# Optimization experiments

Hardware: AMD Instinct MI355X
Metric: run time of the kernel (lower is better)

The kernel has to match this reference:

```python
import jax, jax.numpy as jnp
import numpy as np

HIDDEN = 128
N_HEADS = 8
SEQ = 4096


def setup_inputs() -> dict:
    key = jax.random.key(0)
    ks = jax.random.split(key, 7)
    H, NH = HIDDEN, N_HEADS
    s = 1.0 / np.sqrt(H)
    return {
        "x": jax.random.normal(ks[0], (SEQ, H), dtype=jnp.float32),
        "W1": jax.random.uniform(ks[1], (H, H * NH), jnp.float32, -s, s),
        "b1": jax.random.uniform(ks[2], (H * NH,), jnp.float32, -s, s),
        "W2": jax.random.uniform(ks[3], (H, H * NH), jnp.float32, -s, s),
        "b2": jax.random.uniform(ks[4], (H * NH,), jnp.float32, -s, s),
        "Wc": jax.random.uniform(ks[5], (H * NH, H), jnp.float32, -1.0 / np.sqrt(H * NH), 1.0 / np.sqrt(H * NH)),
        "bc": jax.random.uniform(ks[6], (H,), jnp.float32, -1.0 / np.sqrt(H * NH), 1.0 / np.sqrt(H * NH)),
    }


def reference(x, W1, b1, W2, b2, Wc, bc):
    S, H = x.shape
    NH = W1.shape[1] // H
    # project then split into heads: [S, NH*H] -> [NH, S, H]
    q1 = (x @ W1 + b1).reshape(S, NH, H).transpose(1, 0, 2)
    q2 = (x @ W2 + b2).reshape(S, NH, H).transpose(1, 0, 2)
    # unscaled attention scores per head: [NH, S, S]
    att = jax.nn.softmax(jnp.einsum('hse,hte->hst', q1, q2), axis=-1)
    # weighted sum of q2 (values == q2 in this module): [NH, S, H]
    ctx = jnp.einsum('hst,hte->hse', att, q2)
    # concat heads back along feature dim: [S, NH*H]
    ctx = ctx.transpose(1, 0, 2).reshape(S, NH * H)
    return ctx @ Wc + bc + x
```

## Files before the change

### kernel.cpp

```cpp
#include <hip/hip_runtime.h>

#define H 128
#define NHEADS 8
#define SQ 4096
#define HD 1024

typedef float f32x4 __attribute__((ext_vector_type(4)));
typedef __bf16 bf16x8 __attribute__((ext_vector_type(8)));
typedef unsigned short u16x4 __attribute__((ext_vector_type(4)));
typedef unsigned short u16x8 __attribute__((ext_vector_type(8)));

static __device__ __forceinline__ unsigned short f2bf(float f) {
  unsigned int u = __builtin_bit_cast(unsigned int, f);
  u += 0x7fffu + ((u >> 16) & 1u);
  return (unsigned short)(u >> 16);
}
static __device__ __forceinline__ float b2f(unsigned short s) {
  unsigned int u = (unsigned int)s << 16;
  return __builtin_bit_cast(float, u);
}
static __device__ __forceinline__ bf16x8 ld_bf8(const unsigned short* p) {
  return __builtin_bit_cast(bf16x8, *(const u16x8*)p);
}

__global__ __launch_bounds__(256) void prep_kernel(
    const float* __restrict__ W1, const float* __restrict__ W2,
    const float* __restrict__ Wc,
    unsigned short* __restrict__ W1T, unsigned short* __restrict__ W2T,
    unsigned short* __restrict__ WcT)
{
  __shared__ unsigned short tile[64 * 66];
  const int b = blockIdx.x, tid = threadIdx.x;
  if (b < 32) {
    const int k0 = (b & 1) * 64, n0 = (b >> 1) * 64;
    for (int i = 0; i < 16; ++i) {
      int idx = tid + i * 256;
      int r = idx >> 6, cc = idx & 63;
      tile[cc * 66 + r] = f2bf(W1[(size_t)(k0 + r) * HD + n0 + cc]);
    }
    __syncthreads();
    for (int i = 0; i < 16; ++i) {
      int idx = tid + i * 256;
      int r = idx >> 6, cc = idx & 63;
      W1T[(size_t)(n0 + r) * H + k0 + cc] = tile[r * 66 + cc];
    }
    __syncthreads();
    for (int i = 0; i < 16; ++i) {
      int idx = tid + i * 256;
      int r = idx >> 6, cc = idx & 63;
      tile[cc * 66 + r] = f2bf(W2[(size_t)(k0 + r) * HD + n0 + cc]);
    }
    __syncthreads();
    for (int i = 0; i < 16; ++i) {
      int idx = tid + i * 256;
      int r = idx >> 6, cc = idx & 63;
      W2T[(size_t)(n0 + r) * H + k0 + cc] = tile[r * 66 + cc];
    }
  } else {
    const int bb = b - 32;
    const int n0 = (bb & 1) * 64, k0 = (bb >> 1) * 64;
    for (int i = 0; i < 16; ++i) {
      int idx = tid + i * 256;
      int r = idx >> 6, cc = idx & 63;
      tile[cc * 66 + r] = f2bf(Wc[(size_t)(k0 + r) * H + n0 + cc]);
    }
    __syncthreads();
    for (int i = 0; i < 16; ++i) {
      int idx = tid + i * 256;
      int r = idx >> 6, cc = idx & 63;
      WcT[(size_t)(n0 + r) * HD + k0 + cc] = tile[r * 66 + cc];
    }
  }
}

__global__ __launch_bounds__(256) void proj_kernel(
    const float* __restrict__ x,
    const float* __restrict__ b1, const float* __restrict__ b2,
    const unsigned short* __restrict__ W1T, const unsigned short* __restrict__ W2T,
    unsigned short* __restrict__ q1bf, unsigned short* __restrict__ q2K,
    unsigned short* __restrict__ q2VT)
{
  __shared__ unsigned short At[64 * 136];
  __shared__ unsigned short Bt[128 * 136];
  const int tid = threadIdx.x;
  const int st = blockIdx.x & 63, h = blockIdx.x >> 6;
  const int s0 = st * 64;
  const int lane = tid & 63, w = tid >> 6;
  const int c = lane & 15, q4 = lane >> 4;

  for (int i = 0; i < 4; ++i) {
    int ch = tid + i * 256;
    int row = ch >> 4, col8 = (ch & 15) * 8;
    const float* gp = x + (s0 + row) * H + col8;
    f32x4 a = *(const f32x4*)gp;
    f32x4 b = *(const f32x4*)(gp + 4);
    u16x8 v;
    v[0]=f2bf(a[0]); v[1]=f2bf(a[1]); v[2]=f2bf(a[2]); v[3]=f2bf(a[3]);
    v[4]=f2bf(b[0]); v[5]=f2bf(b[1]); v[6]=f2bf(b[2]); v[7]=f2bf(b[3]);
    *(u16x8*)&At[row * 136 + col8] = v;
  }
  for (int i = 0; i < 8; ++i) {
    int ch = tid + i * 256;
    int row = ch >> 4, col8 = (ch & 15) * 8;
    *(u16x8*)&Bt[row * 136 + col8] = *(const u16x8*)&W1T[(h * H + row) * H + col8];
  }
  __syncthreads();

  bf16x8 af[4];
  for (int kc = 0; kc < 4; ++kc)
    af[kc] = ld_bf8(&At[(w * 16 + c) * 136 + kc * 32 + q4 * 8]);
  __syncthreads();

  for (int nt = 0; nt < 8; ++nt) {
    f32x4 acc = {0.f, 0.f, 0.f, 0.f};
    for (int kc = 0; kc < 4; ++kc) {
      bf16x8 bf = ld_bf8(&Bt[(nt * 16 + c) * 136 + kc * 32 + q4 * 8]);
      acc = __builtin_amdgcn_mfma_f32_16x16x32_bf16(af[kc], bf, acc, 0, 0, 0);
    }
    float bb = b1[h * H + nt * 16 + c];
    for (int r = 0; r < 4; ++r)
      At[(w * 16 + q4 * 4 + r) * 136 + nt * 16 + c] = f2bf(acc[r] + bb);
  }
  __syncthreads();

  for (int i = 0; i < 4; ++i) {
    int ch = tid + i * 256;
    int row = ch >> 4, col8 = (ch & 15) * 8;
    *(u16x8*)&q1bf[(size_t)(h * SQ + s0 + row) * H + col8] =
        *(const u16x8*)&At[row * 136 + col8];
  }
  for (int i = 0; i < 8; ++i) {
    int ch = tid + i * 256;
    int row = ch >> 4, col8 = (ch & 15) * 8;
    *(u16x8*)&Bt[row * 136 + col8] = *(const u16x8*)&W2T[(h * H + row) * H + col8];
  }
  __syncthreads();

  f32x4 q2a[8];
  for (int nt = 0; nt < 8; ++nt) {
    f32x4 acc = {0.f, 0.f, 0.f, 0.f};
    for (int kc = 0; kc < 4; ++kc) {
      bf16x8 bf = ld_bf8(&Bt[(nt * 16 + c) * 136 + kc * 32 + q4 * 8]);
      acc = __builtin_amdgcn_mfma_f32_16x16x32_bf16(af[kc], bf, acc, 0, 0, 0);
    }
    q2a[nt] = acc;
  }
  __syncthreads();

  for (int nt = 0; nt < 8; ++nt) {
    float bb = b2[h * H + nt * 16 + c];
    unsigned short vs[4];
    for (int r = 0; r < 4; ++r) {
      unsigned short u = f2bf(q2a[nt][r] + bb);
      At[(w * 16 + q4 * 4 + r) * 136 + nt * 16 + c] = u;
      vs[r] = u;
    }
    u16x4 v4 = {vs[0], vs[1], vs[2], vs[3]};
    *(u16x4*)&Bt[(nt * 16 + c) * 72 + w * 16 + q4 * 4] = v4;
  }
  __syncthreads();

  for (int i = 0; i < 4; ++i) {
    int ch = tid + i * 256;
    int row = ch >> 4, col8 = (ch & 15) * 8;
    *(u16x8*)&q2K[(size_t)(h * SQ + s0 + row) * H + col8] =
        *(const u16x8*)&At[row * 136 + col8];
  }
  for (int i = 0; i < 4; ++i) {
    int ch = tid + i * 256;
    int row = ch >> 3, col8 = (ch & 7) * 8;
    *(u16x8*)&q2VT[(size_t)(h * H + row) * SQ + s0 + col8] =
        *(const u16x8*)&Bt[row * 72 + col8];
  }
}

__global__ __launch_bounds__(256, 2) void flash_kernel(
    const unsigned short* __restrict__ q1bf,
    const unsigned short* __restrict__ q2K,
    const unsigned short* __restrict__ q2VT,
    unsigned short* __restrict__ ctxp,
    float* __restrict__ lbuf)
{
  __shared__ unsigned short Kt[64 * 152];
  __shared__ unsigned short VT[128 * 88];
  __shared__ unsigned short Pb[4][2][16 * 72];
  const int tid = threadIdx.x;
  const int bid = blockIdx.x;
  const int kb = bid >> 8;
  const int h = (bid >> 5) & 7, qb = bid & 31;
  const int s0 = qb * 128;
  const int kbase = kb * 2048;
  const int lane = tid & 63, w = tid >> 6;
  const int c = lane & 15, q4 = lane >> 4;

  bf16x8 qf[2][4];
  for (int blk = 0; blk < 2; ++blk)
    for (int kc = 0; kc < 4; ++kc)
      qf[blk][kc] = ld_bf8(
          &q1bf[(h * SQ + s0 + w * 32 + blk * 16 + c) * H + kc * 32 + q4 * 8]);

  f32x4 acc[2][8];
  for (int blk = 0; blk < 2; ++blk)
    for (int nt = 0; nt < 8; ++nt) acc[blk][nt] = (f32x4){0.f, 0.f, 0.f, 0.f};
  float lsum[2] = {0.f, 0.f};

  u16x8 kreg[4], vreg[4];
  for (int i = 0; i < 4; ++i) {
    int ch = tid + i * 256;
    kreg[i] = *(const u16x8*)&q2K[(h * SQ + kbase + (ch >> 4)) * H + (ch & 15) * 8];
    vreg[i] = *(const u16x8*)&q2VT[(h * H + (ch >> 3)) * SQ + kbase + (ch & 7) * 8];
  }

  for (int kt = 0; kt < 32; ++kt) {
    if (kt) __syncthreads();
    for (int i = 0; i < 4; ++i) {
      int ch = tid + i * 256;
      *(u16x8*)&Kt[(ch >> 4) * 152 + (ch & 15) * 8] = kreg[i];
      *(u16x8*)&VT[(ch >> 3) * 88 + (ch & 7) * 8] = vreg[i];
    }
    __syncthreads();

    if (kt < 31) {
      const int k0 = kbase + (kt + 1) * 64;
      for (int i = 0; i < 4; ++i) {
        int ch = tid + i * 256;
        kreg[i] = *(const u16x8*)&q2K[(h * SQ + k0 + (ch >> 4)) * H + (ch & 15) * 8];
        vreg[i] = *(const u16x8*)&q2VT[(h * H + (ch >> 3)) * SQ + k0 + (ch & 7) * 8];
      }
    }

    f32x4 sc[2][4];
    for (int mt = 0; mt < 4; ++mt) {
      bf16x8 kf[4];
      for (int kc = 0; kc < 4; ++kc)
        kf[kc] = ld_bf8(&Kt[(mt * 16 + c) * 152 + kc * 32 + q4 * 8]);
      for (int blk = 0; blk < 2; ++blk) {
        f32x4 s = {0.f, 0.f, 0.f, 0.f};
        for (int kc = 0; kc < 4; ++kc)
          s = __builtin_amdgcn_mfma_f32_16x16x32_bf16(kf[kc], qf[blk][kc], s, 0, 0, 0);
        sc[blk][mt] = s;
      }
    }

    for (int blk = 0; blk < 2; ++blk) {
      float ts = 0.f;
      for (int mt = 0; mt < 4; ++mt) {
        f32x4 p;
        for (int r = 0; r < 4; ++r) { p[r] = __expf(sc[blk][mt][r]); ts += p[r]; }
        sc[blk][mt] = p;
      }
      lsum[blk] += ts;
      for (int mt = 0; mt < 4; ++mt) {
        u16x4 pv = {f2bf(sc[blk][mt][0]), f2bf(sc[blk][mt][1]),
                    f2bf(sc[blk][mt][2]), f2bf(sc[blk][mt][3])};
        *(u16x4*)&Pb[w][blk][c * 72 + mt * 16 + q4 * 4] = pv;
      }
    }

    for (int kc2 = 0; kc2 < 2; ++kc2) {
      bf16x8 pf0 = ld_bf8(&Pb[w][0][c * 72 + kc2 * 32 + q4 * 8]);
      bf16x8 pf1 = ld_bf8(&Pb[w][1][c * 72 + kc2 * 32 + q4 * 8]);
      for (int nt = 0; nt < 8; ++nt) {
        bf16x8 vf = ld_bf8(&VT[(nt * 16 + c) * 88 + kc2 * 32 + q4 * 8]);
        acc[0][nt] = __builtin_amdgcn_mfma_f32_16x16x32_bf16(pf0, vf, acc[0][nt], 0, 0, 0);
        acc[1][nt] = __builtin_amdgcn_mfma_f32_16x16x32_bf16(pf1, vf, acc[1][nt], 0, 0, 0);
      }
    }
  }

  unsigned short* ctxk = ctxp + (size_t)kb * SQ * HD;
  for (int blk = 0; blk < 2; ++blk) {
    float l = lsum[blk];
    l += __shfl_xor(l, 16);
    l += __shfl_xor(l, 32);
    float rl = 1.f / l;
    if (q4 == 0)
      lbuf[(size_t)kb * NHEADS * SQ + h * SQ + s0 + w * 32 + blk * 16 + c] = l;
    float r0 = __shfl(rl, q4 * 4 + 0);
    float r1 = __shfl(rl, q4 * 4 + 1);
    float r2 = __shfl(rl, q4 * 4 + 2);
    float r3 = __shfl(rl, q4 * 4 + 3);
    for (int nt = 0; nt < 8; ++nt) {
      int col = h * H + nt * 16 + c;
      int srow = s0 + w * 32 + blk * 16 + q4 * 4;
      ctxk[(size_t)(srow + 0) * HD + col] = f2bf(acc[blk][nt][0] * r0);
      ctxk[(size_t)(srow + 1) * HD + col] = f2bf(acc[blk][nt][1] * r1);
      ctxk[(size_t)(srow + 2) * HD + col] = f2bf(acc[blk][nt][2] * r2);
      ctxk[(size_t)(srow + 3) * HD + col] = f2bf(acc[blk][nt][3] * r3);
    }
  }
}

__global__ __launch_bounds__(256) void out_kernel(
    const unsigned short* __restrict__ ctxp,
    const float* __restrict__ lbuf,
    const unsigned short* __restrict__ WcT,
    const float* __restrict__ bc,
    const float* __restrict__ x,
    float* __restrict__ out)
{
  __shared__ unsigned short At[64 * 136];
  __shared__ unsigned short Bt[128 * 136];
  const int tid = threadIdx.x;
  const int s0 = blockIdx.x * 64;
  const int lane = tid & 63, w = tid >> 6;
  const int c = lane & 15, q4 = lane >> 4;

  f32x4 acc[8];
  for (int nt = 0; nt < 8; ++nt) acc[nt] = (f32x4){0.f, 0.f, 0.f, 0.f};

  for (int kt = 0; kt < 8; ++kt) {
    __syncthreads();
    for (int i = 0; i < 4; ++i) {
      int ch = tid + i * 256;
      int row = ch >> 4, col8 = (ch & 15) * 8;
      const unsigned short* p0 = &ctxp[(size_t)(s0 + row) * HD + kt * 128 + col8];
      u16x8 a0 = *(const u16x8*)p0;
      u16x8 a1 = *(const u16x8*)(p0 + (size_t)SQ * HD);
      float la = lbuf[(size_t)kt * SQ + s0 + row];
      float lb = lbuf[(size_t)NHEADS * SQ + (size_t)kt * SQ + s0 + row];
      float ri = 1.f / (la + lb);
      float wa = la * ri, wb = lb * ri;
      u16x8 av;
      for (int e = 0; e < 8; ++e)
        av[e] = f2bf(wa * b2f(a0[e]) + wb * b2f(a1[e]));
      *(u16x8*)&At[row * 136 + col8] = av;
    }
    for (int i = 0; i < 8; ++i) {
      int ch = tid + i * 256;
      int row = ch >> 4, col8 = (ch & 15) * 8;
      *(u16x8*)&Bt[row * 136 + col8] =
          *(const u16x8*)&WcT[row * HD + kt * 128 + col8];
    }
    __syncthreads();
    bf16x8 af[4];
    for (int kc = 0; kc < 4; ++kc)
      af[kc] = ld_bf8(&At[(w * 16 + c) * 136 + kc * 32 + q4 * 8]);
    for (int nt = 0; nt < 8; ++nt) {
      f32x4 a = acc[nt];
      for (int kc = 0; kc < 4; ++kc) {
        bf16x8 bf = ld_bf8(&Bt[(nt * 16 + c) * 136 + kc * 32 + q4 * 8]);
        a = __builtin_amdgcn_mfma_f32_16x16x32_bf16(af[kc], bf, a, 0, 0, 0);
      }
      acc[nt] = a;
    }
  }
  for (int nt = 0; nt < 8; ++nt) {
    float bb = bc[nt * 16 + c];
    for (int r = 0; r < 4; ++r) {
      int srow = s0 + w * 16 + q4 * 4 + r;
      int col = nt * 16 + c;
      out[srow * H + col] = acc[nt][r] + bb + x[srow * H + col];
    }
  }
}

extern "C" void kernel_launch(void* const* d_in, const int* in_sizes, int n_in,
                              void* d_out, int out_size, void* d_ws, size_t ws_size,
                              hipStream_t stream) {
  const float* x  = (const float*)d_in[0];
  const float* W1 = (const float*)d_in[1];
  const float* b1 = (const float*)d_in[2];
  const float* W2 = (const float*)d_in[3];
  const float* b2 = (const float*)d_in[4];
  const float* Wc = (const float*)d_in[5];
  const float* bc = (const float*)d_in[6];
  float* out = (float*)d_out;

  char* ws = (char*)d_ws;
  unsigned short* q1bf = (unsigned short*)ws; ws += (size_t)NHEADS * SQ * H * 2;
  unsigned short* q2K  = (unsigned short*)ws; ws += (size_t)NHEADS * SQ * H * 2;
  unsigned short* q2VT = (unsigned short*)ws; ws += (size_t)NHEADS * SQ * H * 2;
  unsigned short* ctxp = (unsigned short*)ws; ws += (size_t)2 * SQ * HD * 2;
  float*          lbuf = (float*)ws;          ws += (size_t)2 * NHEADS * SQ * 4;
  unsigned short* W1T  = (unsigned short*)ws; ws += (size_t)HD * H * 2;
  unsigned short* W2T  = (unsigned short*)ws; ws += (size_t)HD * H * 2;
  unsigned short* WcT  = (unsigned short*)ws; ws += (size_t)HD * H * 2;

  prep_kernel<<<64, 256, 0, stream>>>(W1, W2, Wc, W1T, W2T, WcT);
  proj_kernel<<<512, 256, 0, stream>>>(x, b1, b2, W1T, W2T, q1bf, q2K, q2VT);
  flash_kernel<<<512, 256, 0, stream>>>(q1bf, q2K, q2VT, ctxp, lbuf);
  out_kernel<<<64, 256, 0, stream>>>(ctxp, lbuf, WcT, bc, x, out);
}
```

Baseline: 207.1 us.

## Split flash attention keys into three chunks when workspace allows

The flash kernel is templated on the number of key splits. When the workspace is large enough it launches 768 blocks, with each block covering 21 or 22 key tiles, instead of 512 blocks covering 32 tiles each. The output kernel combines the NKB partial results using weights taken from the per-split row sums. LDS row padding is also reduced (152 to 136 for K, 88 to 72 for V), which can change bank conflicts. The extra split adds more partial-context traffic to global memory and more combine work in the output stage.

```diff
diff --git a/kernel.cpp b/kernel.cpp
--- a/kernel.cpp
+++ b/kernel.cpp
@@ -174,22 +174,25 @@
   }
 }
 
-__global__ __launch_bounds__(256, 2) void flash_kernel(
+template<int NKB>
+__global__ __launch_bounds__(256, NKB) void flash_kernel(
     const unsigned short* __restrict__ q1bf,
     const unsigned short* __restrict__ q2K,
     const unsigned short* __restrict__ q2VT,
     unsigned short* __restrict__ ctxp,
     float* __restrict__ lbuf)
 {
-  __shared__ unsigned short Kt[64 * 152];
-  __shared__ unsigned short VT[128 * 88];
+  __shared__ unsigned short Kt[64 * 136];
+  __shared__ unsigned short VT[128 * 72];
   __shared__ unsigned short Pb[4][2][16 * 72];
   const int tid = threadIdx.x;
   const int bid = blockIdx.x;
   const int kb = bid >> 8;
   const int h = (bid >> 5) & 7, qb = bid & 31;
   const int s0 = qb * 128;
-  const int kbase = kb * 2048;
+  const int ntiles = (NKB == 2) ? 32 : (kb == 0 ? 22 : 21);
+  const int kbase = (NKB == 2) ? kb * 2048
+                               : (kb == 0 ? 0 : 1408 + (kb - 1) * 1344);
   const int lane = tid & 63, w = tid >> 6;
   const int c = lane & 15, q4 = lane >> 4;
 
@@ -211,16 +214,16 @@
     vreg[i] = *(const u16x8*)&q2VT[(h * H + (ch >> 3)) * SQ + kbase + (ch & 7) * 8];
   }
 
-  for (int kt = 0; kt < 32; ++kt) {
+  for (int kt = 0; kt < ntiles; ++kt) {
     if (kt) __syncthreads();
     for (int i = 0; i < 4; ++i) {
       int ch = tid + i * 256;
-      *(u16x8*)&Kt[(ch >> 4) * 152 + (ch & 15) * 8] = kreg[i];
-      *(u16x8*)&VT[(ch >> 3) * 88 + (ch & 7) * 8] = vreg[i];
-    }
-    __syncthreads();
-
-    if (kt < 31) {
+      *(u16x8*)&Kt[(ch >> 4) * 136 + (ch & 15) * 8] = kreg[i];
+      *(u16x8*)&VT[(ch >> 3) * 72 + (ch & 7) * 8] = vreg[i];
+    }
+    __syncthreads();
+
+    if (kt < ntiles - 1) {
       const int k0 = kbase + (kt + 1) * 64;
       for (int i = 0; i < 4; ++i) {
         int ch = tid + i * 256;
@@ -233,7 +236,7 @@
     for (int mt = 0; mt < 4; ++mt) {
       bf16x8 kf[4];
       for (int kc = 0; kc < 4; ++kc)
-        kf[kc] = ld_bf8(&Kt[(mt * 16 + c) * 152 + kc * 32 + q4 * 8]);
+        kf[kc] = ld_bf8(&Kt[(mt * 16 + c) * 136 + kc * 32 + q4 * 8]);
       for (int blk = 0; blk < 2; ++blk) {
         f32x4 s = {0.f, 0.f, 0.f, 0.f};
         for (int kc = 0; kc < 4; ++kc)
@@ -261,7 +264,7 @@
       bf16x8 pf0 = ld_bf8(&Pb[w][0][c * 72 + kc2 * 32 + q4 * 8]);
       bf16x8 pf1 = ld_bf8(&Pb[w][1][c * 72 + kc2 * 32 + q4 * 8]);
       for (int nt = 0; nt < 8; ++nt) {
-        bf16x8 vf = ld_bf8(&VT[(nt * 16 + c) * 88 + kc2 * 32 + q4 * 8]);
+        bf16x8 vf = ld_bf8(&VT[(nt * 16 + c) * 72 + kc2 * 32 + q4 * 8]);
         acc[0][nt] = __builtin_amdgcn_mfma_f32_16x16x32_bf16(pf0, vf, acc[0][nt], 0, 0, 0);
         acc[1][nt] = __builtin_amdgcn_mfma_f32_16x16x32_bf16(pf1, vf, acc[1][nt], 0, 0, 0);
       }
@@ -291,6 +294,7 @@
   }
 }
 
+template<int NKB>
 __global__ __launch_bounds__(256) void out_kernel(
     const unsigned short* __restrict__ ctxp,
     const float* __restrict__ lbuf,
@@ -315,15 +319,21 @@
       int ch = tid + i * 256;
       int row = ch >> 4, col8 = (ch & 15) * 8;
       const unsigned short* p0 = &ctxp[(size_t)(s0 + row) * HD + kt * 128 + col8];
-      u16x8 a0 = *(const u16x8*)p0;
-      u16x8 a1 = *(const u16x8*)(p0 + (size_t)SQ * HD);
-      float la = lbuf[(size_t)kt * SQ + s0 + row];
-      float lb = lbuf[(size_t)NHEADS * SQ + (size_t)kt * SQ + s0 + row];
-      float ri = 1.f / (la + lb);
-      float wa = la * ri, wb = lb * ri;
+      float lv[NKB], lsum = 0.f;
+      for (int kb = 0; kb < NKB; ++kb) {
+        lv[kb] = lbuf[(size_t)kb * NHEADS * SQ + (size_t)kt * SQ + s0 + row];
+        lsum += lv[kb];
+      }
+      float ri = 1.f / lsum;
+      float fv[8];
+      for (int e = 0; e < 8; ++e) fv[e] = 0.f;
+      for (int kb = 0; kb < NKB; ++kb) {
+        u16x8 a = *(const u16x8*)(p0 + (size_t)kb * SQ * HD);
+        float wgt = lv[kb] * ri;
+        for (int e = 0; e < 8; ++e) fv[e] += wgt * b2f(a[e]);
+      }
       u16x8 av;
-      for (int e = 0; e < 8; ++e)
-        av[e] = f2bf(wa * b2f(a0[e]) + wb * b2f(a1[e]));
+      for (int e = 0; e < 8; ++e) av[e] = f2bf(fv[e]);
       *(u16x8*)&At[row * 136 + col8] = av;
     }
     for (int i = 0; i < 8; ++i) {
@@ -367,18 +377,29 @@
   const float* bc = (const float*)d_in[6];
   float* out = (float*)d_out;
 
+  const size_t NEED3 = (size_t)3 * NHEADS * SQ * H * 2
+                     + (size_t)3 * SQ * HD * 2
+                     + (size_t)3 * NHEADS * SQ * 4
+                     + (size_t)3 * HD * H * 2;
+  const int nkb = (ws_size >= NEED3) ? 3 : 2;
+
   char* ws = (char*)d_ws;
   unsigned short* q1bf = (unsigned short*)ws; ws += (size_t)NHEADS * SQ * H * 2;
   unsigned short* q2K  = (unsigned short*)ws; ws += (size_t)NHEADS * SQ * H * 2;
   unsigned short* q2VT = (unsigned short*)ws; ws += (size_t)NHEADS * SQ * H * 2;
-  unsigned short* ctxp = (unsigned short*)ws; ws += (size_t)2 * SQ * HD * 2;
-  float*          lbuf = (float*)ws;          ws += (size_t)2 * NHEADS * SQ * 4;
+  unsigned short* ctxp = (unsigned short*)ws; ws += (size_t)nkb * SQ * HD * 2;
+  float*          lbuf = (float*)ws;          ws += (size_t)nkb * NHEADS * SQ * 4;
   unsigned short* W1T  = (unsigned short*)ws; ws += (size_t)HD * H * 2;
   unsigned short* W2T  = (unsigned short*)ws; ws += (size_t)HD * H * 2;
   unsigned short* WcT  = (unsigned short*)ws; ws += (size_t)HD * H * 2;
 
   prep_kernel<<<64, 256, 0, stream>>>(W1, W2, Wc, W1T, W2T, WcT);
   proj_kernel<<<512, 256, 0, stream>>>(x, b1, b2, W1T, W2T, q1bf, q2K, q2VT);
-  flash_kernel<<<512, 256, 0, stream>>>(q1bf, q2K, q2VT, ctxp, lbuf);
-  out_kernel<<<64, 256, 0, stream>>>(ctxp, lbuf, WcT, bc, x, out);
-}
+  if (nkb == 3) {
+    flash_kernel<3><<<768, 256, 0, stream>>>(q1bf, q2K, q2VT, ctxp, lbuf);
+    out_kernel<3><<<64, 256, 0, stream>>>(ctxp, lbuf, WcT, bc, x, out);
+  } else {
+    flash_kernel<2><<<512, 256, 0, stream>>>(q1bf, q2K, q2VT, ctxp, lbuf);
+    out_kernel<2><<<64, 256, 0, stream>>>(ctxp, lbuf, WcT, bc, x, out);
+  }
+}
```

Measured after the change: 343.6 us. 66.0% more time.
